# Kernel optimization log

Hardware: AMD Instinct MI355X
Metric: run time of the kernel (lower is better)

The kernel has to match this reference:

```python
import jax, jax.numpy as jnp
import numpy as np

B, S, D, H, HD, R = 1, 3072, 2048, 16, 128, 16
ALPHA = 16.0
EPS = 1e-6


def _rope_freqs():
    # standard RoPE angles, interleave-duplicated so freqs[..., 0::2] gives the
    # per-pair cos values exactly as the torch module slices them
    inv = 1.0 / (10000.0 ** (np.arange(0, HD, 2, dtype=np.float32) / HD))  # [HD/2]
    ang = np.arange(S, dtype=np.float32)[:, None] * inv[None, :]           # [S, HD/2]
    cos = np.repeat(np.cos(ang), 2, axis=-1).reshape(1, S, 1, HD)
    sin = np.repeat(np.sin(ang), 2, axis=-1).reshape(1, S, 1, HD)
    return jnp.asarray(cos), jnp.asarray(sin)


def setup_inputs() -> dict:
    key = jax.random.key(0)
    ks = jax.random.split(key, 18)
    n = jax.random.normal
    WS = 0.02  # weight init scale
    freqs_cos, freqs_sin = _rope_freqs()
    return {
        "hidden_states": n(ks[0], (B, S, D), jnp.float32),
        "wq": n(ks[1], (D, D), jnp.float32) * WS,
        "bq": n(ks[2], (D,), jnp.float32) * WS,
        "wk": n(ks[3], (D, D), jnp.float32) * WS,
        "bk": n(ks[4], (D,), jnp.float32) * WS,
        "wv": n(ks[5], (D, D), jnp.float32) * WS,
        "bv": n(ks[6], (D,), jnp.float32) * WS,
        "wo": n(ks[7], (D, D), jnp.float32) * WS,
        "bo": n(ks[8], (D,), jnp.float32) * WS,
        "lq_down": n(ks[9], (R, D), jnp.float32) / R,
        "lq_up": n(ks[10], (D, R), jnp.float32) * WS,
        "lk_down": n(ks[11], (R, D), jnp.float32) / R,
        "lk_up": n(ks[12], (D, R), jnp.float32) * WS,
        "lv_down": n(ks[13], (R, D), jnp.float32) / R,
        "lv_up": n(ks[14], (D, R), jnp.float32) * WS,
        "lo_down": n(ks[15], (R, D), jnp.float32) / R,
        "lo_up": n(ks[16], (D, R), jnp.float32) * WS,
        "norm_q_w": jnp.ones((D,), jnp.float32),
        "norm_k_w": jnp.ones((D,), jnp.float32),
        "freqs_cos": freqs_cos,
        "freqs_sin": freqs_sin,
    }


def _lora(x, w_down, w_up, scale):
    return (x @ w_down.T) @ w_up.T * scale


def _rmsnorm(x, w):
    return x * jax.lax.rsqrt(jnp.mean(x * x, axis=-1, keepdims=True) + EPS) * w


def _apply_rotary(x, freqs_cos, freqs_sin):
    # x: [B,S,H,HD]; freqs: [1,S,1,HD]
    x1, x2 = x[..., 0::2], x[..., 1::2]
    c = freqs_cos[..., 0::2]
    s = freqs_sin[..., 1::2]
    even = x1 * c - x2 * s
    odd = x1 * s + x2 * c
    return jnp.stack([even, odd], axis=-1).reshape(x.shape)


def reference(hidden_states, wq, bq, wk, bk, wv, bv, wo, bo,
              lq_down, lq_up, lk_down, lk_up, lv_down, lv_up, lo_down, lo_up,
              norm_q_w, norm_k_w, freqs_cos, freqs_sin):
    scale = ALPHA / R
    x = hidden_states
    # qkv projections + LoRA adds (self-attention: encoder_hidden_states = hidden_states)
    q = x @ wq.T + bq + _lora(x, lq_down, lq_up, scale)
    k = x @ wk.T + bk + _lora(x, lk_down, lk_up, scale)
    v = x @ wv.T + bv + _lora(x, lv_down, lv_up, scale)
    # RMSNorm over full d_model, then split heads
    q = _rmsnorm(q, norm_q_w).reshape(B, S, H, HD)
    k = _rmsnorm(k, norm_k_w).reshape(B, S, H, HD)
    v = v.reshape(B, S, H, HD)
    # custom strided rotary embedding
    q = _apply_rotary(q, freqs_cos, freqs_sin)
    k = _apply_rotary(k, freqs_cos, freqs_sin)
    # SDPA (non-causal, no mask)
    scores = jnp.einsum('bihd,bjhd->bhij', q, k) / jnp.sqrt(jnp.float32(HD))
    attn = jax.nn.softmax(scores, axis=-1)
    o = jnp.einsum('bhij,bjhd->bihd', attn, v).reshape(B, S, D)
    # output projection + LoRA
    out = o @ wo.T + bo + _lora(o, lo_down, lo_up, scale)
    return out
```

## Files before the change

### kernel.cpp

```cpp
#include <hip/hip_runtime.h>
#include <stdint.h>

#define S_LEN 3072
#define DIM   2048
#define NH    16
#define HDIM  128
#define RANK  16
#define EPS_F 1e-6f
#define LORA_SCALE 1.0f
#define QK_SCALE 0.08838834764831845f
#define SM_MAX 24.0f

typedef unsigned short u16;
typedef __attribute__((ext_vector_type(8))) short short8;
typedef __attribute__((ext_vector_type(4))) float f32x4;
typedef __attribute__((ext_vector_type(4))) unsigned short u16x4;
typedef __attribute__((ext_vector_type(8))) unsigned short u16x8;
typedef __attribute__((ext_vector_type(2))) unsigned short u16x2;
typedef __attribute__((ext_vector_type(4))) float float4a;

__device__ __forceinline__ u16 f2b(float f) {
  uint32_t u = __builtin_bit_cast(uint32_t, f);
  u += 0x7fffu + ((u >> 16) & 1u);
  return (u16)(u >> 16);
}
__device__ __forceinline__ u16 f2b_trunc(float f) {
  return (u16)(__builtin_bit_cast(uint32_t, f) >> 16);
}
__device__ __forceinline__ float b2f(u16 b) {
  uint32_t u = ((uint32_t)b) << 16;
  return __builtin_bit_cast(float, u);
}

__device__ __forceinline__ void g2l16(const void* g, void* l) {
  __builtin_amdgcn_global_load_lds(
      (__attribute__((address_space(1))) unsigned int*)g,
      (__attribute__((address_space(3))) unsigned int*)l, 16, 0, 0);
}

__global__ __launch_bounds__(256) void convf2b(const float* __restrict__ in,
                                               u16* __restrict__ out) {
  int i = (blockIdx.x * 256 + threadIdx.x) * 4;
  float4a v = *(const float4a*)(in + i);
  u16x4 o = { f2b(v[0]), f2b(v[1]), f2b(v[2]), f2b(v[3]) };
  *(u16x4*)(out + i) = o;
}

__global__ __launch_bounds__(256) void fold_lora(const float* __restrict__ W,
                                                 const float* __restrict__ lu,
                                                 const float* __restrict__ ld,
                                                 u16* __restrict__ out) {
  __shared__ float lds_ld[16][136];
  __shared__ float lds_lu[64][17];
  const int tid = threadIdx.x;
  const int k0 = blockIdx.x * 128, n0 = blockIdx.y * 64;
  {
    int idx = tid * 8, r = idx >> 7, c = idx & 127;
    const float* src = ld + r * DIM + k0 + c;
#pragma unroll
    for (int e = 0; e < 8; ++e) lds_ld[r][c + e] = src[e];
  }
  {
    int idx = tid * 4, n = idx >> 4, r4 = idx & 15;
    const float* src = lu + (size_t)(n0 + n) * RANK + r4;
#pragma unroll
    for (int e = 0; e < 4; ++e) lds_lu[n][r4 + e] = src[e];
  }
  __syncthreads();
  const int n = tid >> 2;
  const int kg = (tid & 3) * 32;
  float luv[RANK];
#pragma unroll
  for (int r = 0; r < RANK; ++r) luv[r] = lds_lu[n][r];
  const float* wrow = W + (size_t)(n0 + n) * DIM + k0 + kg;
  u16* orow = out + (size_t)(n0 + n) * DIM + k0 + kg;
#pragma unroll
  for (int j = 0; j < 8; ++j) {
    float4a acc = *(const float4a*)(wrow + j * 4);
#pragma unroll
    for (int r = 0; r < RANK; ++r) {
      float4a lv = *(const float4a*)&lds_ld[r][kg + j * 4];
      acc += LORA_SCALE * luv[r] * lv;
    }
    u16x4 o = { f2b(acc[0]), f2b(acc[1]), f2b(acc[2]), f2b(acc[3]) };
    *(u16x4*)(orow + j * 4) = o;
  }
}

template <int TM>
__global__ __launch_bounds__(256, 3) void gemm_core(
    const u16* __restrict__ A, const u16* __restrict__ B,
    const float* __restrict__ b0, const float* __restrict__ b1,
    const float* __restrict__ b2, u16* __restrict__ c0, u16* __restrict__ c1,
    u16* __restrict__ c2, float* __restrict__ Cf) {
  constexpr int WM = TM * 16, BM = 2 * WM;
  __shared__ __attribute__((aligned(16))) u16 As[BM * 64];
  __shared__ __attribute__((aligned(16))) u16 Bs[128 * 64];
  const int tid = threadIdx.x;
  const int wave = tid >> 6, lane = tid & 63;
  const int quad = lane >> 4, l15 = lane & 15;
  const int m0 = blockIdx.x * BM, n0 = blockIdx.y * 128;
  const int mat = n0 >> 11;
  const float* bias = (mat == 0) ? b0 : (mat == 1 ? b1 : b2);
  u16* Cb = (mat == 0) ? c0 : (mat == 1 ? c1 : c2);
  const int wr = wave >> 1, wc = wave & 1;
  f32x4 acc[TM][4] = {};
  for (int kt = 0; kt < DIM / 64; ++kt) {
    __syncthreads();
#pragma unroll
    for (int i = 0; i < TM * 2; ++i) {
      int chunk = i * 256 + tid;
      int row = chunk >> 3, c8 = chunk & 7;
      g2l16(A + (size_t)(m0 + row) * DIM + kt * 64 + c8 * 8,
            As + (i * 256 + wave * 64) * 8);
    }
#pragma unroll
    for (int i = 0; i < 4; ++i) {
      int chunk = i * 256 + tid;
      int row = chunk >> 3, c8 = chunk & 7;
      g2l16(B + (size_t)(n0 + row) * DIM + kt * 64 + c8 * 8,
            Bs + (i * 256 + wave * 64) * 8);
    }
    __syncthreads();
#pragma unroll
    for (int kc = 0; kc < 2; ++kc) {
      short8 af[TM], bf[4];
#pragma unroll
      for (int tm = 0; tm < TM; ++tm)
        af[tm] = *(const short8*)(As + (wr * WM + tm * 16 + l15) * 64 +
                                  kc * 32 + quad * 8);
#pragma unroll
      for (int tn = 0; tn < 4; ++tn)
        bf[tn] = *(const short8*)(Bs + (wc * 64 + tn * 16 + l15) * 64 +
                                  kc * 32 + quad * 8);
#pragma unroll
      for (int tm = 0; tm < TM; ++tm)
#pragma unroll
        for (int tn = 0; tn < 4; ++tn)
          acc[tm][tn] = __builtin_amdgcn_mfma_f32_16x16x32_bf16(
              af[tm], bf[tn], acc[tm][tn], 0, 0, 0);
    }
  }
#pragma unroll
  for (int tn = 0; tn < 4; ++tn) {
    int col = n0 + wc * 64 + tn * 16 + l15;
    int colL = col & (DIM - 1);
    float bcol = bias[colL];
#pragma unroll
    for (int tm = 0; tm < TM; ++tm) {
#pragma unroll
      for (int r = 0; r < 4; ++r) {
        int row = m0 + wr * WM + tm * 16 + quad * 4 + r;
        float val = acc[tm][tn][r] + bcol;
        if (Cf) Cf[(size_t)row * DIM + colL] = val;
        else Cb[(size_t)row * DIM + colL] = f2b(val);
      }
    }
  }
}

__global__ __launch_bounds__(256) void rms_rope(
    u16* __restrict__ q, u16* __restrict__ k,
    const float* __restrict__ nqw, const float* __restrict__ nkw,
    const float* __restrict__ fc, const float* __restrict__ fs) {
  const int s = blockIdx.x, tid = threadIdx.x;
  const int wave = tid >> 6, lane = tid & 63;
  const int e0 = tid * 8;
  u16x8 qa = *(const u16x8*)(q + (size_t)s * DIM + e0);
  u16x8 ka = *(const u16x8*)(k + (size_t)s * DIM + e0);
  float qv[8], kv[8];
  float sq = 0.f, sk = 0.f;
#pragma unroll
  for (int i = 0; i < 8; ++i) {
    qv[i] = b2f(qa[i]); kv[i] = b2f(ka[i]);
    sq += qv[i] * qv[i];
    sk += kv[i] * kv[i];
  }
#pragma unroll
  for (int off = 32; off > 0; off >>= 1) {
    sq += __shfl_down(sq, off);
    sk += __shfl_down(sk, off);
  }
  __shared__ float part[2][4];
  if (lane == 0) { part[0][wave] = sq; part[1][wave] = sk; }
  __syncthreads();
  float sumq = part[0][0] + part[0][1] + part[0][2] + part[0][3];
  float sumk = part[1][0] + part[1][1] + part[1][2] + part[1][3];
  float rq = rsqrtf(sumq * (1.f / DIM) + EPS_F);
  float rk = rsqrtf(sumk * (1.f / DIM) + EPS_F);
  const int fb = e0 & 127;
  float4a fc0 = *(const float4a*)(fc + s * HDIM + fb);
  float4a fc1 = *(const float4a*)(fc + s * HDIM + fb + 4);
  float4a fs0 = *(const float4a*)(fs + s * HDIM + fb);
  float4a fs1 = *(const float4a*)(fs + s * HDIM + fb + 4);
  float4a nq0 = *(const float4a*)(nqw + e0);
  float4a nq1 = *(const float4a*)(nqw + e0 + 4);
  float4a nk0 = *(const float4a*)(nkw + e0);
  float4a nk1 = *(const float4a*)(nkw + e0 + 4);
  float cj[4] = { fc0[0], fc0[2], fc1[0], fc1[2] };
  float sj[4] = { fs0[1], fs0[3], fs1[1], fs1[3] };
  float nq[8] = { nq0[0], nq0[1], nq0[2], nq0[3], nq1[0], nq1[1], nq1[2], nq1[3] };
  float nk[8] = { nk0[0], nk0[1], nk0[2], nk0[3], nk1[0], nk1[1], nk1[2], nk1[3] };
  u16x8 qo, ko;
#pragma unroll
  for (int j = 0; j < 4; ++j) {
    float c = cj[j], sn = sj[j];
    float e = qv[2 * j] * rq * nq[2 * j];
    float o = qv[2 * j + 1] * rq * nq[2 * j + 1];
    qo[2 * j]     = f2b((e * c - o * sn) * QK_SCALE);
    qo[2 * j + 1] = f2b((e * sn + o * c) * QK_SCALE);
    float e2 = kv[2 * j] * rk * nk[2 * j];
    float o2 = kv[2 * j + 1] * rk * nk[2 * j + 1];
    ko[2 * j]     = f2b(e2 * c - o2 * sn);
    ko[2 * j + 1] = f2b(e2 * sn + o2 * c);
  }
  *(u16x8*)(q + (size_t)s * DIM + e0) = qo;
  *(u16x8*)(k + (size_t)s * DIM + e0) = ko;
}

__global__ __launch_bounds__(256) void transpose_v(const u16* __restrict__ in,
                                                   u16* __restrict__ out) {
  __shared__ float tile[64][65];
  const int bs = blockIdx.x * 64;
  const int bd = blockIdx.y * 64;
  const int tid = threadIdx.x;
#pragma unroll
  for (int i = 0; i < 4; ++i) {
    int idx = i * 1024 + tid * 4;
    int r = idx >> 6, c = idx & 63;
    u16x4 v = *(const u16x4*)(in + (size_t)(bs + r) * DIM + bd + c);
    tile[r][c + 0] = b2f(v[0]); tile[r][c + 1] = b2f(v[1]);
    tile[r][c + 2] = b2f(v[2]); tile[r][c + 3] = b2f(v[3]);
  }
  __syncthreads();
#pragma unroll
  for (int i = 0; i < 2; ++i) {
    int cid = i * 256 + tid;
    int dr = cid >> 3, sc = cid & 7;
    u16x8 o;
#pragma unroll
    for (int e = 0; e < 8; ++e) o[e] = f2b(tile[sc * 8 + e][dr]);
    *(u16x8*)(out + (size_t)(bd + dr) * S_LEN + bs + sc * 8) = o;
  }
}

__global__ __launch_bounds__(256, 1) void flash_attn(
    const u16* __restrict__ qb, const u16* __restrict__ kb,
    const u16* __restrict__ vt, u16* __restrict__ ob) {
  __shared__ __attribute__((aligned(16))) u16 Ks[64 * 128];
  __shared__ __attribute__((aligned(16))) u16 Vt[144 * 64];
  __shared__ __attribute__((aligned(16))) u16 Ps[4][3][16 * 64];
  const int tid = threadIdx.x;
  const int wave = tid >> 6, lane = tid & 63;
  const int quad = lane >> 4, l15 = lane & 15;
  const int q0 = blockIdx.x * 192, h = blockIdx.y;
  short8 qf[3][4];
#pragma unroll
  for (int t = 0; t < 3; ++t) {
    int qrow = q0 + wave * 48 + t * 16 + l15;
#pragma unroll
    for (int kc = 0; kc < 4; ++kc)
      qf[t][kc] = *(const short8*)(qb + (size_t)qrow * DIM + h * HDIM +
                                   kc * 32 + quad * 8);
  }
  {
    int idx = tid * 4, d = 128 + (idx >> 6), c = idx & 63;
    u16 fill = (d == 128) ? (u16)0x3F80 : (u16)0;
    u16x4 v = { fill, fill, fill, fill };
    *(u16x4*)(Vt + d * 64 + c) = v;
  }
  f32x4 of[3][9] = {};
  for (int it = 0; it < S_LEN / 64; ++it) {
    const int j0 = it * 64;
    __syncthreads();
#pragma unroll
    for (int i = 0; i < 4; ++i) {
      int slot = i * 256 + tid;
      int j = slot >> 4, csp = slot & 15;
      int cg = csp ^ (j & 7);
      g2l16(kb + (size_t)(j0 + j) * DIM + h * HDIM + cg * 8,
            Ks + (i * 256 + wave * 64) * 8);
    }
#pragma unroll
    for (int i = 0; i < 4; ++i) {
      int slot = i * 256 + tid;
      int d = slot >> 3, cbp = slot & 7;
      int cbg = cbp ^ (d & 7);
      g2l16(vt + (size_t)(h * HDIM + d) * S_LEN + j0 + cbg * 8,
            Vt + (i * 256 + wave * 64) * 8);
    }
    __syncthreads();
    f32x4 sf[3][4] = {};
#pragma unroll
    for (int kc = 0; kc < 4; ++kc) {
#pragma unroll
      for (int tn = 0; tn < 4; ++tn) {
        int j = tn * 16 + l15;
        int csp = (kc * 4 + quad) ^ (j & 7);
        short8 bfr = *(const short8*)(Ks + j * 128 + csp * 8);
#pragma unroll
        for (int t = 0; t < 3; ++t)
          sf[t][tn] = __builtin_amdgcn_mfma_f32_16x16x32_bf16(
              qf[t][kc], bfr, sf[t][tn], 0, 0, 0);
      }
    }
#pragma unroll
    for (int t = 0; t < 3; ++t) {
      u16* pw = &Ps[wave][t][0];
#pragma unroll
      for (int r = 0; r < 4; ++r) {
        int row = quad * 4 + r;
#pragma unroll
        for (int tn = 0; tn < 4; ++tn) {
          float p = __expf(sf[t][tn][r] - SM_MAX);
          int cb = (tn * 2 + (l15 >> 3)) ^ (row & 7);
          pw[row * 64 + cb * 8 + (l15 & 7)] = f2b_trunc(p);
        }
      }
    }
    __syncthreads();
#pragma unroll
    for (int kc2 = 0; kc2 < 2; ++kc2) {
      short8 af[3];
#pragma unroll
      for (int t = 0; t < 3; ++t)
        af[t] = *(const short8*)(&Ps[wave][t][0] + l15 * 64 +
                                 (((kc2 * 4 + quad) ^ (l15 & 7)) * 8));
#pragma unroll
      for (int dt = 0; dt < 9; ++dt) {
        int d = dt * 16 + l15;
        int cb = (kc2 * 4 + quad) ^ (d & 7);
        short8 bfr = *(const short8*)(Vt + d * 64 + cb * 8);
#pragma unroll
        for (int t = 0; t < 3; ++t)
          of[t][dt] = __builtin_amdgcn_mfma_f32_16x16x32_bf16(
              af[t], bfr, of[t][dt], 0, 0, 0);
      }
    }
  }
#pragma unroll
  for (int t = 0; t < 3; ++t) {
#pragma unroll
    for (int r = 0; r < 4; ++r) {
      float li = __shfl(of[t][8][r], lane & 48);
      float inv = 1.f / li;
      int row = q0 + wave * 48 + t * 16 + quad * 4 + r;
#pragma unroll
      for (int dt = 0; dt < 8; ++dt)
        ob[(size_t)row * DIM + h * HDIM + dt * 16 + l15] =
            f2b(of[t][dt][r] * inv);
    }
  }
}

extern "C" void kernel_launch(void* const* d_in, const int* in_sizes, int n_in,
                              void* d_out, int out_size, void* d_ws,
                              size_t ws_size, hipStream_t stream) {
  (void)in_sizes; (void)n_in; (void)out_size; (void)ws_size;
  const float* x   = (const float*)d_in[0];
  const float* wq  = (const float*)d_in[1];
  const float* bq  = (const float*)d_in[2];
  const float* wk  = (const float*)d_in[3];
  const float* bk  = (const float*)d_in[4];
  const float* wv  = (const float*)d_in[5];
  const float* bv  = (const float*)d_in[6];
  const float* wo  = (const float*)d_in[7];
  const float* bo  = (const float*)d_in[8];
  const float* lqd = (const float*)d_in[9];
  const float* lqu = (const float*)d_in[10];
  const float* lkd = (const float*)d_in[11];
  const float* lku = (const float*)d_in[12];
  const float* lvd = (const float*)d_in[13];
  const float* lvu = (const float*)d_in[14];
  const float* lod = (const float*)d_in[15];
  const float* lou = (const float*)d_in[16];
  const float* nqw = (const float*)d_in[17];
  const float* nkw = (const float*)d_in[18];
  const float* fc  = (const float*)d_in[19];
  const float* fs  = (const float*)d_in[20];

  char* ws = (char*)d_ws;
  size_t off = 0;
  auto alloc = [&](size_t bytes) {
    void* p = ws + off;
    off += (bytes + 255) & ~(size_t)255;
    return p;
  };
  const size_t SD2 = (size_t)S_LEN * DIM * 2;
  const size_t WW  = (size_t)DIM * DIM;
  u16* xb    = (u16*)alloc(SD2);
  u16* wqkvb = (u16*)alloc(3 * WW * 2);
  u16* wob   = (u16*)alloc(WW * 2);
  u16* q16   = (u16*)alloc(SD2);
  u16* k16   = (u16*)alloc(SD2);
  u16* v16   = (u16*)alloc(SD2);
  u16* vbT   = (u16*)alloc(SD2);
  u16* ob    = (u16*)alloc(SD2);

  dim3 foldg(DIM / 128, DIM / 64);
  convf2b<<<S_LEN * DIM / 1024, 256, 0, stream>>>(x, xb);
  fold_lora<<<foldg, 256, 0, stream>>>(wq, lqu, lqd, wqkvb);
  fold_lora<<<foldg, 256, 0, stream>>>(wk, lku, lkd, wqkvb + WW);
  fold_lora<<<foldg, 256, 0, stream>>>(wv, lvu, lvd, wqkvb + 2 * WW);
  fold_lora<<<foldg, 256, 0, stream>>>(wo, lou, lod, wob);
  gemm_core<4><<<dim3(S_LEN / 128, 3 * DIM / 128), 256, 0, stream>>>(
      xb, wqkvb, bq, bk, bv, q16, k16, v16, nullptr);
  rms_rope<<<S_LEN, 256, 0, stream>>>(q16, k16, nqw, nkw, fc, fs);
  transpose_v<<<dim3(S_LEN / 64, DIM / 64), 256, 0, stream>>>(v16, vbT);
  flash_attn<<<dim3(S_LEN / 192, NH), 256, 0, stream>>>(q16, k16, vbT, ob);
  gemm_core<2><<<dim3(S_LEN / 64, DIM / 128), 256, 0, stream>>>(
      ob, wob, bo, nullptr, nullptr, nullptr, nullptr, nullptr, (float*)d_out);
}
```

Measured before the change: 501.3 us.

## Double-buffer K/V tiles in flash attention and use smaller blocks

The flash attention kernel moves from 256-thread blocks (192 query rows) to 128-thread blocks (96 query rows) with two blocks per CU, and double-buffers the K and V shared-memory tiles so the next tile's global-to-LDS copy is issued before the current tile's compute. The second barrier per iteration becomes an lgkmcnt wait, since each wave only reads back its own P tile. The ones row used to compute the softmax denominator moves into a separate constant LDS buffer. The aim is to hide load latency and cut barrier stalls, at the cost of more LDS per block and twice as many blocks re-reading K/V.

```diff
diff --git a/kernel.cpp b/kernel.cpp
--- a/kernel.cpp
+++ b/kernel.cpp
@@ -244,16 +244,18 @@
   }
 }
 
-__global__ __launch_bounds__(256, 1) void flash_attn(
+__global__ __launch_bounds__(128, 2) void flash_attn(
     const u16* __restrict__ qb, const u16* __restrict__ kb,
     const u16* __restrict__ vt, u16* __restrict__ ob) {
-  __shared__ __attribute__((aligned(16))) u16 Ks[64 * 128];
-  __shared__ __attribute__((aligned(16))) u16 Vt[144 * 64];
-  __shared__ __attribute__((aligned(16))) u16 Ps[4][3][16 * 64];
+  __shared__ __attribute__((aligned(16))) u16 Ks[2][64 * 128];
+  __shared__ __attribute__((aligned(16))) u16 Vt[2][128 * 64];
+  __shared__ __attribute__((aligned(16))) u16 Vones[16 * 64];
+  __shared__ __attribute__((aligned(16))) u16 Ps[2][3][16 * 64];
   const int tid = threadIdx.x;
   const int wave = tid >> 6, lane = tid & 63;
   const int quad = lane >> 4, l15 = lane & 15;
-  const int q0 = blockIdx.x * 192, h = blockIdx.y;
+  const int h = blockIdx.x & 15;
+  const int q0 = (blockIdx.x >> 4) * 96;
   short8 qf[3][4];
 #pragma unroll
   for (int t = 0; t < 3; ++t) {
@@ -264,32 +266,36 @@
                                    kc * 32 + quad * 8);
   }
   {
-    int idx = tid * 4, d = 128 + (idx >> 6), c = idx & 63;
-    u16 fill = (d == 128) ? (u16)0x3F80 : (u16)0;
-    u16x4 v = { fill, fill, fill, fill };
-    *(u16x4*)(Vt + d * 64 + c) = v;
-  }
-  f32x4 of[3][9] = {};
-  for (int it = 0; it < S_LEN / 64; ++it) {
-    const int j0 = it * 64;
-    __syncthreads();
-#pragma unroll
-    for (int i = 0; i < 4; ++i) {
-      int slot = i * 256 + tid;
+    int idx = tid * 8, r = idx >> 6, c = idx & 63;
+    u16 fill = (r == 0) ? (u16)0x3F80 : (u16)0;
+    u16x8 v = { fill, fill, fill, fill, fill, fill, fill, fill };
+    *(u16x8*)(Vones + r * 64 + c) = v;
+  }
+  auto stage = [&](int tile, int buf) {
+    const int j0 = tile * 64;
+#pragma unroll
+    for (int i = 0; i < 8; ++i) {
+      int slot = i * 128 + tid;
       int j = slot >> 4, csp = slot & 15;
       int cg = csp ^ (j & 7);
       g2l16(kb + (size_t)(j0 + j) * DIM + h * HDIM + cg * 8,
-            Ks + (i * 256 + wave * 64) * 8);
-    }
-#pragma unroll
-    for (int i = 0; i < 4; ++i) {
-      int slot = i * 256 + tid;
+            &Ks[buf][(i * 128 + wave * 64) * 8]);
+    }
+#pragma unroll
+    for (int i = 0; i < 8; ++i) {
+      int slot = i * 128 + tid;
       int d = slot >> 3, cbp = slot & 7;
       int cbg = cbp ^ (d & 7);
       g2l16(vt + (size_t)(h * HDIM + d) * S_LEN + j0 + cbg * 8,
-            Vt + (i * 256 + wave * 64) * 8);
-    }
+            &Vt[buf][(i * 128 + wave * 64) * 8]);
+    }
+  };
+  stage(0, 0);
+  f32x4 of[3][9] = {};
+  for (int it = 0; it < S_LEN / 64; ++it) {
+    const int cur = it & 1;
     __syncthreads();
+    if (it + 1 < S_LEN / 64) stage(it + 1, cur ^ 1);
     f32x4 sf[3][4] = {};
 #pragma unroll
     for (int kc = 0; kc < 4; ++kc) {
@@ -297,7 +303,7 @@
       for (int tn = 0; tn < 4; ++tn) {
         int j = tn * 16 + l15;
         int csp = (kc * 4 + quad) ^ (j & 7);
-        short8 bfr = *(const short8*)(Ks + j * 128 + csp * 8);
+        short8 bfr = *(const short8*)(&Ks[cur][j * 128 + csp * 8]);
 #pragma unroll
         for (int t = 0; t < 3; ++t)
           sf[t][tn] = __builtin_amdgcn_mfma_f32_16x16x32_bf16(
@@ -318,7 +324,7 @@
         }
       }
     }
-    __syncthreads();
+    __asm__ volatile("s_waitcnt lgkmcnt(0)" ::: "memory");
 #pragma unroll
     for (int kc2 = 0; kc2 < 2; ++kc2) {
       short8 af[3];
@@ -328,9 +334,13 @@
                                  (((kc2 * 4 + quad) ^ (l15 & 7)) * 8));
 #pragma unroll
       for (int dt = 0; dt < 9; ++dt) {
-        int d = dt * 16 + l15;
-        int cb = (kc2 * 4 + quad) ^ (d & 7);
-        short8 bfr = *(const short8*)(Vt + d * 64 + cb * 8);
+        const short8 bfr =
+            (dt < 8)
+                ? *(const short8*)(&Vt[cur][(dt * 16 + l15) * 64 +
+                                            (((kc2 * 4 + quad) ^
+                                              ((dt * 16 + l15) & 7)) *
+                                             8)])
+                : *(const short8*)(&Vones[l15 * 64 + (kc2 * 4 + quad) * 8]);
 #pragma unroll
         for (int t = 0; t < 3; ++t)
           of[t][dt] = __builtin_amdgcn_mfma_f32_16x16x32_bf16(
@@ -407,7 +417,7 @@
       xb, wqkvb, bq, bk, bv, q16, k16, v16, nullptr);
   rms_rope<<<S_LEN, 256, 0, stream>>>(q16, k16, nqw, nkw, fc, fs);
   transpose_v<<<dim3(S_LEN / 64, DIM / 64), 256, 0, stream>>>(v16, vbT);
-  flash_attn<<<dim3(S_LEN / 192, NH), 256, 0, stream>>>(q16, k16, vbT, ob);
+  flash_attn<<<dim3((S_LEN / 96) * NH), 128, 0, stream>>>(q16, k16, vbT, ob);
   gemm_core<2><<<dim3(S_LEN / 64, DIM / 128), 256, 0, stream>>>(
       ob, wob, bo, nullptr, nullptr, nullptr, nullptr, nullptr, (float*)d_out);
 }
```

After: 490.3 us. -2.2%, faster.
